# Kernel optimization log

Hardware: AMD Instinct MI355X
Metric: run time of the kernel (lower is better)

Reference implementation:

```python
import jax, jax.numpy as jnp
import numpy as np

B, N, E, DIN, DH = 32, 2000, 64000, 128, 128


def setup_inputs() -> dict:
    key = jax.random.key(0)
    ks = jax.random.split(key, 8)
    gene_emb = jax.random.normal(ks[0], (B, N, DIN), dtype=jnp.float32)
    edge_src = jax.random.randint(ks[1], (E,), 0, N, dtype=jnp.int32)
    edge_dst = jax.random.randint(ks[2], (E,), 0, N, dtype=jnp.int32)
    s1 = 1.0 / np.sqrt(DIN)
    s2 = 1.0 / np.sqrt(DH)
    W1 = jax.random.normal(ks[3], (DIN, DH), dtype=jnp.float32) * s1
    b1 = jnp.zeros((DH,), dtype=jnp.float32)
    W2 = jax.random.normal(ks[4], (DH, DH), dtype=jnp.float32) * s2
    b2 = jnp.zeros((DH,), dtype=jnp.float32)
    return {"gene_emb": gene_emb, "edge_src": edge_src, "edge_dst": edge_dst,
            "W1": W1, "b1": b1, "W2": W2, "b2": b2, "pathway_idx": 0}


def _gcn_conv(x, src, dst, norm_e, self_norm, W, b):
    # x: [B, N, Din] -> [B, N, Dout]; PyG GCNConv: linear first, then normalized aggregation
    h = jnp.einsum('bnd,de->bne', x, W)
    msgs = h[:, src, :] * norm_e[None, :, None]          # [B, E, Dout] gather
    agg = jax.vmap(lambda m: jax.ops.segment_sum(m, dst, num_segments=h.shape[1]))(msgs)
    # self-loop contribution (A+I): norm = dinv[i]^2
    return agg + h * self_norm[None, :, None] + b


def reference(gene_emb, edge_src, edge_dst, W1, b1, W2, b2, pathway_idx):
    n = gene_emb.shape[1]
    # symmetric GCN normalization with self loops: deg[i] = in_degree + 1
    deg = jnp.zeros((n,), dtype=gene_emb.dtype).at[edge_dst].add(1.0) + 1.0
    dinv = jax.lax.rsqrt(deg)
    norm_e = dinv[edge_src] * dinv[edge_dst]
    self_norm = dinv * dinv
    x = jax.nn.relu(_gcn_conv(gene_emb, edge_src, edge_dst, norm_e, self_norm, W1, b1))
    x = _gcn_conv(x, edge_src, edge_dst, norm_e, self_norm, W2, b2)
    # global_mean_pool over each graph copy (all graphs have n nodes)
    return jnp.mean(x, axis=1)  # [B, DH]
```

## Files before the change

### kernel.cpp

```cpp
#include <hip/hip_runtime.h>

namespace {
constexpr int NB = 32;
constexpr int NN = 2000;
constexpr int NE = 64000;
constexpr int ND = 128;
constexpr int TR = 32;
constexpr int NCHUNK = (NN + TR - 1) / TR;
constexpr int NXCD = 8;
constexpr int BPB = 2;
constexpr int PAIRS = NB / (NXCD * BPB);
constexpr int GRID_FUSED = NXCD * PAIRS * NCHUNK;
constexpr int SL = 80;
constexpr int ECAP = 1536;

constexpr int CVT_BLOCKS  = 8000;
constexpr int W_BLOCKS    = 8;
constexpr int EDGE_BLOCKS = 250;

constexpr size_t OFF_CNT  = 0;
constexpr size_t OFF_WSUM = OFF_CNT + 2048 * 4;
constexpr size_t OFF_SLOT = OFF_WSUM + 2048 * 4;
constexpr size_t OFF_WF   = OFF_SLOT + (size_t)NN * SL * 4;
constexpr size_t OFF_XBF  = OFF_WF + 32768;
constexpr size_t OFF_YP   = OFF_XBF + (size_t)NB * NN * ND * 2;
constexpr size_t MEMSET_BYTES = 2048 * 4 * 2;

typedef __attribute__((ext_vector_type(8))) short bf16x8;
typedef __attribute__((ext_vector_type(4))) float f32x4;

__device__ __forceinline__ ushort f32_to_bf16(float f) {
    uint u = __float_as_uint(f);
    u += 0x7fffu + ((u >> 16) & 1u);
    return (ushort)(u >> 16);
}
__device__ __forceinline__ uint pack_bf16x2(float lo, float hi) {
    return (uint)f32_to_bf16(lo) | ((uint)f32_to_bf16(hi) << 16);
}
}

__global__ void k_fill(const float* __restrict__ X, ushort* __restrict__ xbf,
                       const float* __restrict__ W1, uint* __restrict__ wf,
                       const int* __restrict__ src, const int* __restrict__ dst,
                       int* __restrict__ cnt, int* __restrict__ slot) {
    const int blk = blockIdx.x;
    if (blk < CVT_BLOCKS) {
        int i = blk * 256 + threadIdx.x;
        float4 v = ((const float4*)X)[i];
        ushort4 o;
        o.x = f32_to_bf16(v.x);
        o.y = f32_to_bf16(v.y);
        o.z = f32_to_bf16(v.z);
        o.w = f32_to_bf16(v.w);
        ((ushort4*)xbf)[i] = o;
    } else if (blk < CVT_BLOCKS + W_BLOCKS) {
        int g = (blk - CVT_BLOCKS) * 256 + threadIdx.x;
        int lane = g & 63, f = g >> 6;
        int nt = f >> 2, kc = f & 3;
        int col = nt * 16 + (lane & 15);
        int k0  = kc * 32 + (lane >> 4) * 8;
        uint4 o;
        o.x = pack_bf16x2(W1[(k0 + 0) * ND + col], W1[(k0 + 1) * ND + col]);
        o.y = pack_bf16x2(W1[(k0 + 2) * ND + col], W1[(k0 + 3) * ND + col]);
        o.z = pack_bf16x2(W1[(k0 + 4) * ND + col], W1[(k0 + 5) * ND + col]);
        o.w = pack_bf16x2(W1[(k0 + 6) * ND + col], W1[(k0 + 7) * ND + col]);
        ((uint4*)wf)[g] = o;
    } else {
        int e = (blk - CVT_BLOCKS - W_BLOCKS) * 256 + threadIdx.x;
        int s = src[e], d = dst[e];
        int p = atomicAdd(&cnt[d], 1);
        if (p < SL) slot[d * SL + p] = s;
    }
}

__global__ void k_wsum(const int* __restrict__ src, const int* __restrict__ dst,
                       const int* __restrict__ cnt, float* __restrict__ wsum) {
    int e = blockIdx.x * 256 + threadIdx.x;
    if (e < NE) {
        int s = src[e], d = dst[e];
        float w = rsqrtf((float)(cnt[s] + 1)) * rsqrtf((float)(cnt[d] + 1));
        atomicAdd(&wsum[s], w);
    }
}

__global__ __launch_bounds__(256, 4) void k_fused(const ushort* __restrict__ xbf,
                                                  const int* __restrict__ cnt,
                                                  const int* __restrict__ slot,
                                                  const float* __restrict__ wsum,
                                                  const uint* __restrict__ wfrag,
                                                  const float* __restrict__ b1,
                                                  float* __restrict__ ypart) {
    __shared__ uint  AsU[2][32 * 68];
    __shared__ int2  sEdge[ECAP];
    __shared__ int   sCnt[32];
    __shared__ int   sBase[33];
    __shared__ float sDinv[32];
    __shared__ float sWn[32];
    __shared__ float yred[2][128];
    const int tid = threadIdx.x;

    const int L     = blockIdx.x;
    const int xcd   = L & (NXCD - 1);
    const int sl    = L >> 3;
    const int pair  = sl / NCHUNK;
    const int chunk = sl % NCHUNK;
    const int b0    = xcd * (BPB * PAIRS) + pair * BPB;
    const int n0    = chunk * TR;

    if (tid < 32) {
        int n = n0 + tid;
        int cr = (n < NN) ? cnt[n] : 0;
        float d = rsqrtf((float)(cr + 1));
        sCnt[tid]  = min(cr, SL);
        sDinv[tid] = d;
        sWn[tid]   = (n < NN) ? (wsum[n] + d * d) : 0.f;
    }
    if (tid < 128) { yred[0][tid] = 0.f; yred[1][tid] = 0.f; }
    __syncthreads();
    if (tid == 0) {
        int s = 0;
        for (int j = 0; j < 32; j++) { sBase[j] = s; s += sCnt[j]; }
        sBase[32] = s;
    }
    __syncthreads();
    const bool staged = (sBase[32] <= ECAP);

    const int wv = tid >> 6, ln = tid & 63;
    if (staged) {
        for (int ii = 0; ii < 8; ii++) {
            int j = wv * 8 + ii;
            int c = sCnt[j];
            float dd = sDinv[j];
            const int* sp = &slot[(size_t)(n0 + j) * SL];
            for (int base = 0; base < c; base += 64) {
                if (base + ln < c) {
                    int sidx = sp[base + ln];
                    float w = rsqrtf((float)(cnt[sidx] + 1)) * dd;
                    sEdge[sBase[j] + base + ln] = make_int2(sidx, __float_as_int(w));
                }
            }
        }
    }
    __syncthreads();

    const uint* __restrict__ Xu0 = (const uint*)(xbf + (size_t)b0 * NN * ND);
    const uint* __restrict__ Xu1 = (const uint*)(xbf + (size_t)(b0 + 1) * NN * ND);
    #pragma unroll 1
    for (int ii = 0; ii < 8; ii++) {
        const int j = wv * 8 + ii;
        const int n = n0 + j;
        float2 a0 = make_float2(0.f, 0.f), a1 = a0, a0b = a0, a1b = a0;
        if (n < NN) {
            float sn = sDinv[j]; sn *= sn;
            uint u0 = Xu0[n * 64 + ln], u1 = Xu1[n * 64 + ln];
            a0.x = sn * __uint_as_float(u0 << 16);
            a0.y = sn * __uint_as_float(u0 & 0xffff0000u);
            a1.x = sn * __uint_as_float(u1 << 16);
            a1.y = sn * __uint_as_float(u1 & 0xffff0000u);
            const int c = sCnt[j];
            if (staged) {
                const int e0 = sBase[j], e1 = e0 + c;
                int e = e0;
                for (; e + 8 <= e1; e += 8) {
                    int sidx[8]; float w[8]; uint q0[8], q1[8];
                    #pragma unroll
                    for (int q = 0; q < 8; q++) {
                        int2 ed = sEdge[e + q];
                        sidx[q] = ed.x; w[q] = __int_as_float(ed.y);
                    }
                    #pragma unroll
                    for (int q = 0; q < 8; q++) {
                        q0[q] = Xu0[sidx[q] * 64 + ln];
                        q1[q] = Xu1[sidx[q] * 64 + ln];
                    }
                    #pragma unroll
                    for (int q = 0; q < 8; q++) {
                        float x0l = __uint_as_float(q0[q] << 16);
                        float x0h = __uint_as_float(q0[q] & 0xffff0000u);
                        float x1l = __uint_as_float(q1[q] << 16);
                        float x1h = __uint_as_float(q1[q] & 0xffff0000u);
                        if (q & 1) {
                            a0b.x = fmaf(w[q], x0l, a0b.x);
                            a0b.y = fmaf(w[q], x0h, a0b.y);
                            a1b.x = fmaf(w[q], x1l, a1b.x);
                            a1b.y = fmaf(w[q], x1h, a1b.y);
                        } else {
                            a0.x = fmaf(w[q], x0l, a0.x);
                            a0.y = fmaf(w[q], x0h, a0.y);
                            a1.x = fmaf(w[q], x1l, a1.x);
                            a1.y = fmaf(w[q], x1h, a1.y);
                        }
                    }
                }
                for (; e < e1; e++) {
                    int2 ed = sEdge[e];
                    float w = __int_as_float(ed.y);
                    uint u0e = Xu0[ed.x * 64 + ln], u1e = Xu1[ed.x * 64 + ln];
                    a0.x = fmaf(w, __uint_as_float(u0e << 16), a0.x);
                    a0.y = fmaf(w, __uint_as_float(u0e & 0xffff0000u), a0.y);
                    a1.x = fmaf(w, __uint_as_float(u1e << 16), a1.x);
                    a1.y = fmaf(w, __uint_as_float(u1e & 0xffff0000u), a1.y);
                }
            } else {
                const int* sp = &slot[(size_t)n * SL];
                float dd = sDinv[j];
                for (int e = 0; e < c; e++) {
                    int sidx = sp[e];
                    float w = rsqrtf((float)(cnt[sidx] + 1)) * dd;
                    uint u0e = Xu0[sidx * 64 + ln], u1e = Xu1[sidx * 64 + ln];
                    a0.x = fmaf(w, __uint_as_float(u0e << 16), a0.x);
                    a0.y = fmaf(w, __uint_as_float(u0e & 0xffff0000u), a0.y);
                    a1.x = fmaf(w, __uint_as_float(u1e << 16), a1.x);
                    a1.y = fmaf(w, __uint_as_float(u1e & 0xffff0000u), a1.y);
                }
            }
            a0.x += a0b.x; a0.y += a0b.y;
            a1.x += a1b.x; a1.y += a1b.y;
        }
        AsU[0][j * 68 + ln] = pack_bf16x2(a0.x, a0.y);
        AsU[1][j * 68 + ln] = pack_bf16x2(a1.x, a1.y);
    }
    __syncthreads();

    const int lane15 = ln & 15, quad = ln >> 4;
    f32x4 zero4 = {0.f, 0.f, 0.f, 0.f};
    f32x4 acc[2][2][2];
    #pragma unroll
    for (int b = 0; b < 2; b++)
        #pragma unroll
        for (int mt = 0; mt < 2; mt++)
            #pragma unroll
            for (int nt2 = 0; nt2 < 2; nt2++) acc[b][mt][nt2] = zero4;

    bf16x8 wf[2][4];
    const bf16x8* Wf8 = (const bf16x8*)wfrag;
    #pragma unroll
    for (int nt2 = 0; nt2 < 2; nt2++)
        #pragma unroll
        for (int kc = 0; kc < 4; kc++)
            wf[nt2][kc] = Wf8[(((2 * wv + nt2) * 4 + kc) * 64) + ln];

    const bf16x8* A8_0 = (const bf16x8*)AsU[0];
    const bf16x8* A8_1 = (const bf16x8*)AsU[1];
    #pragma unroll
    for (int mt = 0; mt < 2; mt++) {
        const int r = mt * 16 + lane15;
        #pragma unroll
        for (int kc = 0; kc < 4; kc++) {
            bf16x8 af0 = A8_0[r * 17 + kc * 4 + quad];
            bf16x8 af1 = A8_1[r * 17 + kc * 4 + quad];
            #pragma unroll
            for (int nt2 = 0; nt2 < 2; nt2++) {
                acc[0][mt][nt2] = __builtin_amdgcn_mfma_f32_16x16x32_bf16(
                    af0, wf[nt2][kc], acc[0][mt][nt2], 0, 0, 0);
                acc[1][mt][nt2] = __builtin_amdgcn_mfma_f32_16x16x32_bf16(
                    af1, wf[nt2][kc], acc[1][mt][nt2], 0, 0, 0);
            }
        }
    }

    #pragma unroll
    for (int nt2 = 0; nt2 < 2; nt2++) {
        int cg = (2 * wv + nt2) * 16 + lane15;
        float bias = b1[cg];
        #pragma unroll
        for (int b = 0; b < 2; b++) {
            float part = 0.f;
            #pragma unroll
            for (int mt = 0; mt < 2; mt++) {
                f32x4 a = acc[b][mt][nt2];
                #pragma unroll
                for (int r = 0; r < 4; r++) {
                    int m = mt * 16 + quad * 4 + r;
                    part = fmaf(sWn[m], fmaxf(a[r] + bias, 0.f), part);
                }
            }
            atomicAdd(&yred[b][cg], part);
        }
    }
    __syncthreads();
    if (tid < 128)
        ypart[((size_t)b0 * NCHUNK + chunk) * ND + tid] = yred[0][tid];
    else
        ypart[((size_t)(b0 + 1) * NCHUNK + chunk) * ND + (tid - 128)] = yred[1][tid - 128];
}

__global__ __launch_bounds__(128) void k_out(const float* __restrict__ ypart,
                                             const float* __restrict__ W2,
                                             const float* __restrict__ b2,
                                             float* __restrict__ out) {
    __shared__ float ys[128];
    const int b = blockIdx.x;
    const int d = threadIdx.x;
    float s = 0.f;
    for (int c = 0; c < NCHUNK; c++)
        s += ypart[((size_t)b * NCHUNK + c) * ND + d];
    ys[d] = s * (1.f / (float)NN);
    __syncthreads();
    float acc = b2[d];
    #pragma unroll 8
    for (int k = 0; k < 128; k++)
        acc = fmaf(ys[k], W2[k * ND + d], acc);
    out[b * ND + d] = acc;
}

extern "C" void kernel_launch(void* const* d_in, const int* in_sizes, int n_in,
                              void* d_out, int out_size, void* d_ws, size_t ws_size,
                              hipStream_t stream) {
    (void)in_sizes; (void)n_in; (void)out_size; (void)ws_size;
    const float* X   = (const float*)d_in[0];
    const int*   src = (const int*)d_in[1];
    const int*   dst = (const int*)d_in[2];
    const float* W1  = (const float*)d_in[3];
    const float* b1  = (const float*)d_in[4];
    const float* W2  = (const float*)d_in[5];
    const float* b2  = (const float*)d_in[6];
    float* out = (float*)d_out;

    char* ws = (char*)d_ws;
    int*    cnt   = (int*)   (ws + OFF_CNT);
    float*  wsum  = (float*) (ws + OFF_WSUM);
    int*    slot  = (int*)   (ws + OFF_SLOT);
    uint*   wfb   = (uint*)  (ws + OFF_WF);
    ushort* xbf   = (ushort*)(ws + OFF_XBF);
    float*  ypart = (float*) (ws + OFF_YP);

    (void)hipMemsetAsync(ws, 0, MEMSET_BYTES, stream);
    k_fill<<<CVT_BLOCKS + W_BLOCKS + EDGE_BLOCKS, 256, 0, stream>>>(
        X, xbf, W1, wfb, src, dst, cnt, slot);
    k_wsum<<<EDGE_BLOCKS, 256, 0, stream>>>(src, dst, cnt, wsum);
    k_fused<<<GRID_FUSED, 256, 0, stream>>>(xbf, cnt, slot, wsum, wfb, b1, ypart);
    k_out<<<NB, 128, 0, stream>>>(ypart, W2, b2, out);
}
```

Measured before the change: 164.6 us.

## Collapse pipeline to two launches with per-node edge lists and last-block epilogue

Removes the memset, the separate wsum kernel and the output kernel. Each node block now scans the full edge list and builds in- and out-adjacency slots with shared-memory atomics, so no global atomics or zero-initialisation are needed. The fused kernel recomputes each node's out-weight sum from the out-slots, accumulates pooled results with global atomics, and lets the last block (chosen by a ticket counter) run the final W2 projection. This cuts launch and dependency overhead, but 250 blocks each reread all 64k edges, and the final matvec now runs serially in a single block.

```diff
diff --git a/kernel.cpp b/kernel.cpp
--- a/kernel.cpp
+++ b/kernel.cpp
@@ -15,16 +15,18 @@
 constexpr int ECAP = 1536;
 
 constexpr int CVT_BLOCKS  = 8000;
+constexpr int NODE_BLOCKS = 250;
 constexpr int W_BLOCKS    = 8;
-constexpr int EDGE_BLOCKS = 250;
+constexpr int PREP_GRID   = CVT_BLOCKS + NODE_BLOCKS + W_BLOCKS;
 
 constexpr size_t OFF_CNT  = 0;
-constexpr size_t OFF_WSUM = OFF_CNT + 2048 * 4;
-constexpr size_t OFF_SLOT = OFF_WSUM + 2048 * 4;
-constexpr size_t OFF_WF   = OFF_SLOT + (size_t)NN * SL * 4;
+constexpr size_t OFF_OCNT = 8192;
+constexpr size_t OFF_Y    = 16384;
+constexpr size_t OFF_DONE = 32768;
+constexpr size_t OFF_SLI  = 32832;
+constexpr size_t OFF_SLO  = OFF_SLI + (size_t)NN * SL * 4;
+constexpr size_t OFF_WF   = OFF_SLO + (size_t)NN * SL * 4;
 constexpr size_t OFF_XBF  = OFF_WF + 32768;
-constexpr size_t OFF_YP   = OFF_XBF + (size_t)NB * NN * ND * 2;
-constexpr size_t MEMSET_BYTES = 2048 * 4 * 2;
 
 typedef __attribute__((ext_vector_type(8))) short bf16x8;
 typedef __attribute__((ext_vector_type(4))) float f32x4;
@@ -39,13 +41,16 @@
 }
 }
 
-__global__ void k_fill(const float* __restrict__ X, ushort* __restrict__ xbf,
+__global__ void k_prep(const float* __restrict__ X, ushort* __restrict__ xbf,
                        const float* __restrict__ W1, uint* __restrict__ wf,
                        const int* __restrict__ src, const int* __restrict__ dst,
-                       int* __restrict__ cnt, int* __restrict__ slot) {
+                       int* __restrict__ cnt, int* __restrict__ ocnt,
+                       int* __restrict__ slot_in, int* __restrict__ slot_out,
+                       float* __restrict__ y, int* __restrict__ done) {
     const int blk = blockIdx.x;
+    const int tid = threadIdx.x;
     if (blk < CVT_BLOCKS) {
-        int i = blk * 256 + threadIdx.x;
+        int i = blk * 256 + tid;
         float4 v = ((const float4*)X)[i];
         ushort4 o;
         o.x = f32_to_bf16(v.x);
@@ -53,8 +58,38 @@
         o.z = f32_to_bf16(v.z);
         o.w = f32_to_bf16(v.w);
         ((ushort4*)xbf)[i] = o;
-    } else if (blk < CVT_BLOCKS + W_BLOCKS) {
-        int g = (blk - CVT_BLOCKS) * 256 + threadIdx.x;
+    } else if (blk < CVT_BLOCKS + NODE_BLOCKS) {
+        const int base = (blk - CVT_BLOCKS) * 8;
+        __shared__ int lcin[8], lcout[8];
+        if (tid < 8) { lcin[tid] = 0; lcout[tid] = 0; }
+        __syncthreads();
+        const int4* s4p = (const int4*)src;
+        const int4* d4p = (const int4*)dst;
+        for (int i = tid; i < NE / 4; i += 256) {
+            int4 s4 = s4p[i], d4 = d4p[i];
+            int ss[4] = {s4.x, s4.y, s4.z, s4.w};
+            int dd[4] = {d4.x, d4.y, d4.z, d4.w};
+            #pragma unroll
+            for (int q = 0; q < 4; q++) {
+                int j = dd[q] - base;
+                if ((unsigned)j < 8u) {
+                    int p = atomicAdd(&lcin[j], 1);
+                    if (p < SL) slot_in[(size_t)dd[q] * SL + p] = ss[q];
+                }
+                int j2 = ss[q] - base;
+                if ((unsigned)j2 < 8u) {
+                    int p2 = atomicAdd(&lcout[j2], 1);
+                    if (p2 < SL) slot_out[(size_t)ss[q] * SL + p2] = dd[q];
+                }
+            }
+        }
+        __syncthreads();
+        if (tid < 8) {
+            cnt[base + tid]  = lcin[tid];
+            ocnt[base + tid] = lcout[tid];
+        }
+    } else {
+        int g = (blk - CVT_BLOCKS - NODE_BLOCKS) * 256 + tid;
         int lane = g & 63, f = g >> 6;
         int nt = f >> 2, kc = f & 3;
         int col = nt * 16 + (lane & 15);
@@ -65,31 +100,23 @@
         o.z = pack_bf16x2(W1[(k0 + 4) * ND + col], W1[(k0 + 5) * ND + col]);
         o.w = pack_bf16x2(W1[(k0 + 6) * ND + col], W1[(k0 + 7) * ND + col]);
         ((uint4*)wf)[g] = o;
-    } else {
-        int e = (blk - CVT_BLOCKS - W_BLOCKS) * 256 + threadIdx.x;
-        int s = src[e], d = dst[e];
-        int p = atomicAdd(&cnt[d], 1);
-        if (p < SL) slot[d * SL + p] = s;
-    }
-}
-
-__global__ void k_wsum(const int* __restrict__ src, const int* __restrict__ dst,
-                       const int* __restrict__ cnt, float* __restrict__ wsum) {
-    int e = blockIdx.x * 256 + threadIdx.x;
-    if (e < NE) {
-        int s = src[e], d = dst[e];
-        float w = rsqrtf((float)(cnt[s] + 1)) * rsqrtf((float)(cnt[d] + 1));
-        atomicAdd(&wsum[s], w);
+        y[2 * g] = 0.f; y[2 * g + 1] = 0.f;
+        if (g == 0) *done = 0;
     }
 }
 
 __global__ __launch_bounds__(256, 4) void k_fused(const ushort* __restrict__ xbf,
                                                   const int* __restrict__ cnt,
-                                                  const int* __restrict__ slot,
-                                                  const float* __restrict__ wsum,
+                                                  const int* __restrict__ ocnt,
+                                                  const int* __restrict__ slot_in,
+                                                  const int* __restrict__ slot_out,
                                                   const uint* __restrict__ wfrag,
                                                   const float* __restrict__ b1,
-                                                  float* __restrict__ ypart) {
+                                                  float* __restrict__ y,
+                                                  int* __restrict__ done,
+                                                  const float* __restrict__ W2,
+                                                  const float* __restrict__ b2,
+                                                  float* __restrict__ out) {
     __shared__ uint  AsU[2][32 * 68];
     __shared__ int2  sEdge[ECAP];
     __shared__ int   sCnt[32];
@@ -97,6 +124,7 @@
     __shared__ float sDinv[32];
     __shared__ float sWn[32];
     __shared__ float yred[2][128];
+    __shared__ int   sTicket;
     const int tid = threadIdx.x;
 
     const int L     = blockIdx.x;
@@ -110,10 +138,8 @@
     if (tid < 32) {
         int n = n0 + tid;
         int cr = (n < NN) ? cnt[n] : 0;
-        float d = rsqrtf((float)(cr + 1));
         sCnt[tid]  = min(cr, SL);
-        sDinv[tid] = d;
-        sWn[tid]   = (n < NN) ? (wsum[n] + d * d) : 0.f;
+        sDinv[tid] = rsqrtf((float)(cr + 1));
     }
     if (tid < 128) { yred[0][tid] = 0.f; yred[1][tid] = 0.f; }
     __syncthreads();
@@ -122,16 +148,36 @@
         for (int j = 0; j < 32; j++) { sBase[j] = s; s += sCnt[j]; }
         sBase[32] = s;
     }
+
+    const int wv = tid >> 6, ln = tid & 63;
+
+    for (int ii = 0; ii < 8; ii++) {
+        const int j = wv * 8 + ii;
+        const int n = n0 + j;
+        float part = 0.f;
+        if (n < NN) {
+            int oc = min(ocnt[n], SL);
+            const int* op = &slot_out[(size_t)n * SL];
+            for (int base = 0; base < oc; base += 64)
+                if (base + ln < oc)
+                    part += rsqrtf((float)(cnt[op[base + ln]] + 1));
+        }
+        #pragma unroll
+        for (int off = 32; off; off >>= 1) part += __shfl_down(part, off, 64);
+        if (ln == 0) {
+            float d = sDinv[j];
+            sWn[j] = (n < NN) ? d * (d + part) : 0.f;
+        }
+    }
     __syncthreads();
     const bool staged = (sBase[32] <= ECAP);
 
-    const int wv = tid >> 6, ln = tid & 63;
     if (staged) {
         for (int ii = 0; ii < 8; ii++) {
             int j = wv * 8 + ii;
             int c = sCnt[j];
             float dd = sDinv[j];
-            const int* sp = &slot[(size_t)(n0 + j) * SL];
+            const int* sp = &slot_in[(size_t)(n0 + j) * SL];
             for (int base = 0; base < c; base += 64) {
                 if (base + ln < c) {
                     int sidx = sp[base + ln];
@@ -202,7 +248,7 @@
                     a1.y = fmaf(w, __uint_as_float(u1e & 0xffff0000u), a1.y);
                 }
             } else {
-                const int* sp = &slot[(size_t)n * SL];
+                const int* sp = &slot_in[(size_t)n * SL];
                 float dd = sDinv[j];
                 for (int e = 0; e < c; e++) {
                     int sidx = sp[e];
@@ -232,13 +278,13 @@
             #pragma unroll
             for (int nt2 = 0; nt2 < 2; nt2++) acc[b][mt][nt2] = zero4;
 
-    bf16x8 wf[2][4];
+    bf16x8 wfr[2][4];
     const bf16x8* Wf8 = (const bf16x8*)wfrag;
     #pragma unroll
     for (int nt2 = 0; nt2 < 2; nt2++)
         #pragma unroll
         for (int kc = 0; kc < 4; kc++)
-            wf[nt2][kc] = Wf8[(((2 * wv + nt2) * 4 + kc) * 64) + ln];
+            wfr[nt2][kc] = Wf8[(((2 * wv + nt2) * 4 + kc) * 64) + ln];
 
     const bf16x8* A8_0 = (const bf16x8*)AsU[0];
     const bf16x8* A8_1 = (const bf16x8*)AsU[1];
@@ -252,9 +298,9 @@
             #pragma unroll
             for (int nt2 = 0; nt2 < 2; nt2++) {
                 acc[0][mt][nt2] = __builtin_amdgcn_mfma_f32_16x16x32_bf16(
-                    af0, wf[nt2][kc], acc[0][mt][nt2], 0, 0, 0);
+                    af0, wfr[nt2][kc], acc[0][mt][nt2], 0, 0, 0);
                 acc[1][mt][nt2] = __builtin_amdgcn_mfma_f32_16x16x32_bf16(
-                    af1, wf[nt2][kc], acc[1][mt][nt2], 0, 0, 0);
+                    af1, wfr[nt2][kc], acc[1][mt][nt2], 0, 0, 0);
             }
         }
     }
@@ -279,29 +325,31 @@
         }
     }
     __syncthreads();
-    if (tid < 128)
-        ypart[((size_t)b0 * NCHUNK + chunk) * ND + tid] = yred[0][tid];
-    else
-        ypart[((size_t)(b0 + 1) * NCHUNK + chunk) * ND + (tid - 128)] = yred[1][tid - 128];
-}
-
-__global__ __launch_bounds__(128) void k_out(const float* __restrict__ ypart,
-                                             const float* __restrict__ W2,
-                                             const float* __restrict__ b2,
-                                             float* __restrict__ out) {
-    __shared__ float ys[128];
-    const int b = blockIdx.x;
-    const int d = threadIdx.x;
-    float s = 0.f;
-    for (int c = 0; c < NCHUNK; c++)
-        s += ypart[((size_t)b * NCHUNK + c) * ND + d];
-    ys[d] = s * (1.f / (float)NN);
-    __syncthreads();
-    float acc = b2[d];
-    #pragma unroll 8
-    for (int k = 0; k < 128; k++)
-        acc = fmaf(ys[k], W2[k * ND + d], acc);
-    out[b * ND + d] = acc;
+    if (tid < 128) atomicAdd(&y[b0 * ND + tid], yred[0][tid]);
+    else           atomicAdd(&y[(b0 + 1) * ND + (tid - 128)], yred[1][tid - 128]);
+
+    asm volatile("s_waitcnt vmcnt(0)" ::: "memory");
+    __syncthreads();
+    if (tid == 0)
+        sTicket = __hip_atomic_fetch_add(done, 1, __ATOMIC_RELAXED,
+                                         __HIP_MEMORY_SCOPE_AGENT);
+    __syncthreads();
+    if (sTicket == GRID_FUSED - 1) {
+        float* ysh = (float*)AsU;
+        for (int i = tid; i < NB * ND; i += 256)
+            ysh[i] = __hip_atomic_load(&y[i], __ATOMIC_RELAXED,
+                                       __HIP_MEMORY_SCOPE_AGENT) * (1.f / (float)NN);
+        __syncthreads();
+        for (int o = tid; o < NB * ND; o += 256) {
+            int bb = o >> 7, d = o & 127;
+            float accO = b2[d];
+            const float* yb = ysh + bb * 128;
+            #pragma unroll 8
+            for (int k = 0; k < 128; k++)
+                accO = fmaf(yb[k], W2[k * ND + d], accO);
+            out[o] = accO;
+        }
+    }
 }
 
 extern "C" void kernel_launch(void* const* d_in, const int* in_sizes, int n_in,
@@ -318,17 +366,17 @@
     float* out = (float*)d_out;
 
     char* ws = (char*)d_ws;
-    int*    cnt   = (int*)   (ws + OFF_CNT);
-    float*  wsum  = (float*) (ws + OFF_WSUM);
-    int*    slot  = (int*)   (ws + OFF_SLOT);
-    uint*   wfb   = (uint*)  (ws + OFF_WF);
-    ushort* xbf   = (ushort*)(ws + OFF_XBF);
-    float*  ypart = (float*) (ws + OFF_YP);
-
-    (void)hipMemsetAsync(ws, 0, MEMSET_BYTES, stream);
-    k_fill<<<CVT_BLOCKS + W_BLOCKS + EDGE_BLOCKS, 256, 0, stream>>>(
-        X, xbf, W1, wfb, src, dst, cnt, slot);
-    k_wsum<<<EDGE_BLOCKS, 256, 0, stream>>>(src, dst, cnt, wsum);
-    k_fused<<<GRID_FUSED, 256, 0, stream>>>(xbf, cnt, slot, wsum, wfb, b1, ypart);
-    k_out<<<NB, 128, 0, stream>>>(ypart, W2, b2, out);
-}
+    int*    cnt  = (int*)   (ws + OFF_CNT);
+    int*    ocnt = (int*)   (ws + OFF_OCNT);
+    float*  y    = (float*) (ws + OFF_Y);
+    int*    done = (int*)   (ws + OFF_DONE);
+    int*    sli  = (int*)   (ws + OFF_SLI);
+    int*    slo  = (int*)   (ws + OFF_SLO);
+    uint*   wfb  = (uint*)  (ws + OFF_WF);
+    ushort* xbf  = (ushort*)(ws + OFF_XBF);
+
+    k_prep<<<PREP_GRID, 256, 0, stream>>>(X, xbf, W1, wfb, src, dst,
+                                          cnt, ocnt, sli, slo, y, done);
+    k_fused<<<GRID_FUSED, 256, 0, stream>>>(xbf, cnt, ocnt, sli, slo, wfb, b1,
+                                            y, done, W2, b2, out);
+}
```

After: 219.4 us. 33.3% more time.
